# Kernel optimization log

Measured on AMD Instinct MI355X. Metric: run time of the kernel, lower is better.

Reference implementation:

```python
import jax, jax.numpy as jnp
import numpy as np

ALPHA = 0.2  # LeakyReLU negative slope
N_NODES = 50000
N_EDGES = 800000
IN_F = 128
OUT_F = 64


def setup_inputs() -> dict:
    key = jax.random.key(0)
    k1, k2, k3, k4 = jax.random.split(key, 4)
    x = jax.random.normal(k1, (N_NODES, IN_F), dtype=jnp.float32)
    edge_index = jax.random.randint(k2, (2, N_EDGES), 0, N_NODES, dtype=jnp.int64)
    # xavier_uniform-ish scales
    W = jax.random.uniform(k3, (IN_F, OUT_F), dtype=jnp.float32,
                           minval=-1.0, maxval=1.0) * (1.414 * np.sqrt(6.0 / (IN_F + OUT_F)))
    a = jax.random.uniform(k4, (2 * OUT_F, 1), dtype=jnp.float32,
                           minval=-1.0, maxval=1.0) * (1.414 * np.sqrt(6.0 / (2 * OUT_F + 1)))
    return {"x": x, "edge_index": edge_index, "W": W, "a": a}


def reference(x, edge_index, W, a):
    Wh = x @ W                               # [N, F_out]
    src = edge_index[0]
    dst = edge_index[1]
    Wh_src = Wh[src]                         # [E, F_out] gather
    Wh_dst = Wh[dst]                         # [E, F_out] gather
    # concat([Wh_src, Wh_dst]) @ a == Wh_src @ a_top + Wh_dst @ a_bot
    F_out = Wh.shape[1]
    a_top = a[:F_out, 0]
    a_bot = a[F_out:, 0]
    e = jax.nn.leaky_relu(Wh_src @ a_top + Wh_dst @ a_bot, negative_slope=ALPHA)  # [E]
    # NOTE: original normalizes softmax over ALL edges (dim=0), not per node.
    attention = jax.nn.softmax(e)            # [E]
    # dropout skipped (eval mode, deterministic reference)
    msgs = Wh_dst * attention[:, None]       # [E, F_out]
    h_prime = jax.ops.segment_sum(msgs, src, num_segments=Wh.shape[0])  # scatter-add
    return jax.nn.elu(h_prime)
```

## Files before the change

kernel.cpp:

```cpp
#include <hip/hip_runtime.h>
#include <math.h>

#define N_NODES 50000
#define N_EDGES 800000
#define IN_F 128
#define OUT_F 64
#define LRELU_ALPHA 0.2f

#define NPB 64
#define NBUCK ((N_NODES + NPB - 1) / NPB)
#define EPT 16
#define NBT ((N_EDGES / EPT + 255) / 256)
#define CHUNK 2048

typedef __attribute__((ext_vector_type(8))) short bf16x8;
typedef __attribute__((ext_vector_type(4))) float f32x4;

__device__ inline float wred_sum(float v) {
#pragma unroll
    for (int o = 32; o > 0; o >>= 1) v += __shfl_down(v, o, 64);
    return v;
}

__device__ inline unsigned bf16r(float f) {
    unsigned u = __float_as_uint(f);
    u += 0x7fffu + ((u >> 16) & 1u);
    return u >> 16;
}

__global__ __launch_bounds__(256, 4) void k_wh(const float* __restrict__ x,
                                               const float* __restrict__ W,
                                               const float* __restrict__ a,
                                               const int* __restrict__ src,
                                               unsigned short* __restrict__ Whb,
                                               float* __restrict__ sv,
                                               float* __restrict__ tv,
                                               int* __restrict__ bcnt) {
    __shared__ unsigned short xb[64 * 128];
    __shared__ unsigned short wtl[64 * 128];
    __shared__ float wt_s[128], wb_s[128];
    __shared__ int hc[NBUCK];

    const int tid = threadIdx.x;
    const int row0 = blockIdx.x * 64;

    for (int i = tid; i < NBUCK; i += 256) hc[i] = 0;

    for (int i = tid; i < 2048; i += 256) {
        int k = i >> 4, c4 = (i & 15) << 2;
        float4 wv = *reinterpret_cast<const float4*>(W + k * 64 + c4);
        int kb = k >> 3, kr = k & 7;
        wtl[(c4 + 0) * 128 + ((kb ^ ((c4 + 0) & 15)) << 3) + kr] = (unsigned short)bf16r(wv.x);
        wtl[(c4 + 1) * 128 + ((kb ^ ((c4 + 1) & 15)) << 3) + kr] = (unsigned short)bf16r(wv.y);
        wtl[(c4 + 2) * 128 + ((kb ^ ((c4 + 2) & 15)) << 3) + kr] = (unsigned short)bf16r(wv.z);
        wtl[(c4 + 3) * 128 + ((kb ^ ((c4 + 3) & 15)) << 3) + kr] = (unsigned short)bf16r(wv.w);
    }

    if (tid < 128) {
        int k = tid;
        float s = 0.0f, t = 0.0f;
#pragma unroll
        for (int c4 = 0; c4 < 64; c4 += 4) {
            float4 wv = *reinterpret_cast<const float4*>(W + k * 64 + c4);
            float4 at = *reinterpret_cast<const float4*>(a + c4);
            float4 ab = *reinterpret_cast<const float4*>(a + 64 + c4);
            s = fmaf(wv.w, at.w, fmaf(wv.z, at.z, fmaf(wv.y, at.y, fmaf(wv.x, at.x, s))));
            t = fmaf(wv.w, ab.w, fmaf(wv.z, ab.z, fmaf(wv.y, ab.y, fmaf(wv.x, ab.x, t))));
        }
        wt_s[k] = s;
        wb_s[k] = t;
    }

    {
        int j0 = blockIdx.x * 1024 + tid * 4;
        if (j0 < N_EDGES) {
            int4 s4 = *reinterpret_cast<const int4*>(src + j0);
            atomicAdd(&hc[s4.x >> 6], 1);
            atomicAdd(&hc[s4.y >> 6], 1);
            atomicAdd(&hc[s4.z >> 6], 1);
            atomicAdd(&hc[s4.w >> 6], 1);
        }
    }
    __syncthreads();

    const int cc = (tid & 31) << 2;
    float4 wt4 = *reinterpret_cast<const float4*>(wt_s + cc);
    float4 wb4 = *reinterpret_cast<const float4*>(wb_s + cc);
    float ps[8], pt[8];
#pragma unroll
    for (int it = 0; it < 8; ++it) {
        int i = tid + it * 256;
        int rl = i >> 5;
        int r = row0 + rl;
        float4 v = make_float4(0.f, 0.f, 0.f, 0.f);
        if (r < N_NODES) v = *reinterpret_cast<const float4*>(x + (size_t)r * IN_F + cc);
        ps[it] = fmaf(v.w, wt4.w, fmaf(v.z, wt4.z, fmaf(v.y, wt4.y, v.x * wt4.x)));
        pt[it] = fmaf(v.w, wb4.w, fmaf(v.z, wb4.z, fmaf(v.y, wb4.y, v.x * wb4.x)));
        int kb = cc >> 3;
        uint2 pk;
        pk.x = bf16r(v.x) | (bf16r(v.y) << 16);
        pk.y = bf16r(v.z) | (bf16r(v.w) << 16);
        *reinterpret_cast<uint2*>(
            &xb[rl * 128 + (kb ^ (rl & 15)) * 8 + ((cc >> 2) & 1) * 4]) = pk;
    }
    __syncthreads();

    const int l = tid & 63, w = tid >> 6;
    const int rloc0 = w * 16;
    const int arow = rloc0 + (l & 15);
    const int kgrp = l >> 4;
    f32x4 acc[4] = {f32x4{0,0,0,0}, f32x4{0,0,0,0}, f32x4{0,0,0,0}, f32x4{0,0,0,0}};
#pragma unroll
    for (int t = 0; t < 4; ++t) {
        int kb = t * 4 + kgrp;
        bf16x8 af = *reinterpret_cast<const bf16x8*>(
            &xb[arow * 128 + (kb ^ (arow & 15)) * 8]);
#pragma unroll
        for (int ct = 0; ct < 4; ++ct) {
            int brow = ct * 16 + (l & 15);
            bf16x8 bfr = *reinterpret_cast<const bf16x8*>(
                &wtl[brow * 128 + (kb ^ (brow & 15)) * 8]);
            acc[ct] = __builtin_amdgcn_mfma_f32_16x16x32_bf16(af, bfr, acc[ct], 0, 0, 0);
        }
    }

#pragma unroll
    for (int ct = 0; ct < 4; ++ct) {
#pragma unroll
        for (int i = 0; i < 4; ++i) {
            int r = row0 + rloc0 + (l >> 4) * 4 + i;
            if (r < N_NODES)
                Whb[(size_t)r * OUT_F + ct * 16 + (l & 15)] =
                    (unsigned short)bf16r(acc[ct][i]);
        }
    }

#pragma unroll
    for (int it = 0; it < 8; ++it) {
        float s = ps[it], t2 = pt[it];
#pragma unroll
        for (int o = 1; o < 32; o <<= 1) {
            s += __shfl_xor(s, o, 64);
            t2 += __shfl_xor(t2, o, 64);
        }
        int r = row0 + (tid >> 5) + it * 8;
        if ((tid & 31) == 0 && r < N_NODES) { sv[r] = s; tv[r] = t2; }
    }

    for (int i = tid; i < NBUCK; i += 256) {
        int v = hc[i];
        if (v) atomicAdd(&bcnt[i], v);
    }
}

__global__ __launch_bounds__(1024) void k_bscan(const int* __restrict__ bcnt,
                                                int* __restrict__ bbase,
                                                int* __restrict__ cursor) {
    __shared__ int wsum[16], woff[16];
    int t = threadIdx.x, lane = t & 63, w = t >> 6;
    int c = (t < NBUCK) ? bcnt[t] : 0;
    int run = c;
#pragma unroll
    for (int o = 1; o < 64; o <<= 1) {
        int v = __shfl_up(run, o, 64);
        if (lane >= o) run += v;
    }
    if (lane == 63) wsum[w] = run;
    __syncthreads();
    if (t == 0) {
        int r = 0;
#pragma unroll
        for (int i = 0; i < 16; i++) { woff[i] = r; r += wsum[i]; }
    }
    __syncthreads();
    int ex = run - c + woff[w];
    if (t < NBUCK) {
        bbase[t] = ex;
        cursor[t] = ex;
    }
    if (t == 0) bbase[NBUCK] = N_EDGES;
}

__global__ __launch_bounds__(256) void k_binscatter(const int* __restrict__ src,
                                                    const int* __restrict__ dst,
                                                    const float* __restrict__ sv,
                                                    const float* __restrict__ tv,
                                                    int* __restrict__ cursor,
                                                    int2* __restrict__ rec,
                                                    float* __restrict__ psum) {
    __shared__ int lcnt[NBUCK];
    __shared__ int lbase[NBUCK];
    const int tid = threadIdx.x;
    for (int i = tid; i < NBUCK; i += 256) lcnt[i] = 0;
    __syncthreads();

    int t = blockIdx.x * 256 + tid;
    int j0 = t * EPT;
    bool ok = (j0 < N_EDGES);

    int s_[EPT], d_[EPT], rk[EPT];
    float ev[EPT];
    float lsum = 0.0f;
    if (ok) {
#pragma unroll
        for (int q = 0; q < 4; q++) {
            int4 s4 = *reinterpret_cast<const int4*>(src + j0 + q * 4);
            int4 d4 = *reinterpret_cast<const int4*>(dst + j0 + q * 4);
            s_[q * 4 + 0] = s4.x; s_[q * 4 + 1] = s4.y;
            s_[q * 4 + 2] = s4.z; s_[q * 4 + 3] = s4.w;
            d_[q * 4 + 0] = d4.x; d_[q * 4 + 1] = d4.y;
            d_[q * 4 + 2] = d4.z; d_[q * 4 + 3] = d4.w;
        }
        float svv[EPT], tvv[EPT];
#pragma unroll
        for (int k = 0; k < EPT; k++) svv[k] = sv[s_[k]];
#pragma unroll
        for (int k = 0; k < EPT; k++) tvv[k] = tv[d_[k]];
#pragma unroll
        for (int k = 0; k < EPT; k++) {
            float vv = svv[k] + tvv[k];
            vv = vv > 0.0f ? vv : LRELU_ALPHA * vv;
            float e = __expf(vv);
            ev[k] = e;
            lsum += e;
        }
#pragma unroll
        for (int k = 0; k < EPT; k++) rk[k] = atomicAdd(&lcnt[s_[k] >> 6], 1);
    }
    __syncthreads();

    for (int i = tid; i < NBUCK; i += 256) {
        int c = lcnt[i];
        lbase[i] = c ? atomicAdd(&cursor[i], c) : 0;
    }
    __syncthreads();

    if (ok) {
#pragma unroll
        for (int k = 0; k < EPT; k++) {
            int b = s_[k] >> 6;
            rec[lbase[b] + rk[k]] =
                make_int2(d_[k] | ((s_[k] & (NPB - 1)) << 16), __float_as_int(ev[k]));
        }
    }

    float wsum = wred_sum(lsum);
    __shared__ float rsm[4];
    if ((tid & 63) == 0) rsm[tid >> 6] = wsum;
    __syncthreads();
    if (tid == 0)
        psum[blockIdx.x] = rsm[0] + rsm[1] + rsm[2] + rsm[3];
}

__global__ __launch_bounds__(512) void k_bgather(const int* __restrict__ bbase,
                                                 const int2* __restrict__ rec,
                                                 const float* __restrict__ psum,
                                                 const unsigned short* __restrict__ Whb,
                                                 float* __restrict__ out) {
    __shared__ int2 sorted[CHUNK];
    __shared__ int scnt[NPB], soff[NPB], shead[NPB];
    __shared__ float ginv_s;

    const int tid = threadIdx.x;
    const int lane = tid & 63, w = tid >> 6;
    const int j = lane & 31, h = lane >> 5;
    const int b = blockIdx.x;
    const int e0 = bbase[b], e1 = bbase[b + 1];

    if (tid < 64) {
        float lsum = 0.0f;
        for (int i = tid; i < NBT; i += 64) lsum += psum[i];
        float ws = wred_sum(lsum);
        if (tid == 0) ginv_s = 1.0f / ws;
    }
    __syncthreads();
    const float ginv = ginv_s;

    float ax[8], ay[8];
#pragma unroll
    for (int k = 0; k < 8; k++) { ax[k] = 0.0f; ay[k] = 0.0f; }

    for (int base = e0; base < e1; base += CHUNK) {
        int m = e1 - base;
        if (m > CHUNK) m = CHUNK;

        int2 rr[4];
        int ln[4];
        bool vv[4];
        if (tid < NPB) scnt[tid] = 0;
        __syncthreads();
#pragma unroll
        for (int q = 0; q < 4; q++) {
            int idx = tid + q * 512;
            vv[q] = idx < m;
            rr[q] = make_int2(0, 0);
            ln[q] = 0;
            if (vv[q]) {
                rr[q] = rec[base + idx];
                ln[q] = (rr[q].x >> 16) & (NPB - 1);
                atomicAdd(&scnt[ln[q]], 1);
            }
        }
        __syncthreads();

        if (tid < 64) {
            int c = scnt[tid];
            int run = c;
#pragma unroll
            for (int o = 1; o < 64; o <<= 1) {
                int src_ln = (tid >= o) ? (tid - o) : tid;
                int t2 = __shfl(run, src_ln, 64);
                if (tid >= o) run += t2;
            }
            int excl = run - c;
            soff[tid] = excl;
            shead[tid] = excl;
        }
        __syncthreads();

#pragma unroll
        for (int q = 0; q < 4; q++) {
            if (vv[q]) {
                int pos = atomicAdd(&shead[ln[q]], 1);
                sorted[pos] = make_int2(rr[q].x & 0xFFFF, rr[q].y);
            }
        }
        __syncthreads();

#pragma unroll
        for (int k = 0; k < 8; k++) {
            int node = w * 8 + k;
            int lo = soff[node], c = scnt[node];
            float px = 0.0f, py = 0.0f;
            int i = 0;
            for (; i + 7 < c; i += 8) {
                int2 q0 = sorted[lo + i + h];
                int2 q1 = sorted[lo + i + 2 + h];
                int2 q2 = sorted[lo + i + 4 + h];
                int2 q3 = sorted[lo + i + 6 + h];
                const unsigned* p0 =
                    reinterpret_cast<const unsigned*>(Whb + (size_t)q0.x * OUT_F);
                const unsigned* p1 =
                    reinterpret_cast<const unsigned*>(Whb + (size_t)q1.x * OUT_F);
                const unsigned* p2 =
                    reinterpret_cast<const unsigned*>(Whb + (size_t)q2.x * OUT_F);
                const unsigned* p3 =
                    reinterpret_cast<const unsigned*>(Whb + (size_t)q3.x * OUT_F);
                unsigned u0 = p0[j];
                unsigned u1 = p1[j];
                unsigned u2 = p2[j];
                unsigned u3 = p3[j];
                float att0 = __int_as_float(q0.y);
                float att1 = __int_as_float(q1.y);
                float att2 = __int_as_float(q2.y);
                float att3 = __int_as_float(q3.y);
                px = fmaf(att0, __uint_as_float((u0 & 0xffffu) << 16), px);
                py = fmaf(att0, __uint_as_float(u0 & 0xffff0000u), py);
                px = fmaf(att1, __uint_as_float((u1 & 0xffffu) << 16), px);
                py = fmaf(att1, __uint_as_float(u1 & 0xffff0000u), py);
                px = fmaf(att2, __uint_as_float((u2 & 0xffffu) << 16), px);
                py = fmaf(att2, __uint_as_float(u2 & 0xffff0000u), py);
                px = fmaf(att3, __uint_as_float((u3 & 0xffffu) << 16), px);
                py = fmaf(att3, __uint_as_float(u3 & 0xffff0000u), py);
            }
            for (; i < c; i += 2) {
                int ii = i + h;
                bool val = ii < c;
                int2 q = sorted[lo + (val ? ii : i)];
                const unsigned* p =
                    reinterpret_cast<const unsigned*>(Whb + (size_t)q.x * OUT_F);
                unsigned u = p[j];
                float att = val ? __int_as_float(q.y) : 0.0f;
                px = fmaf(att, __uint_as_float((u & 0xffffu) << 16), px);
                py = fmaf(att, __uint_as_float(u & 0xffff0000u), py);
            }
            ax[k] += px;
            ay[k] += py;
        }
        __syncthreads();
    }

#pragma unroll
    for (int k = 0; k < 8; k++) {
        float sx = ax[k] + __shfl_down(ax[k], 32, 64);
        float sy = ay[k] + __shfl_down(ay[k], 32, 64);
        int n = b * NPB + w * 8 + k;
        if (h == 0 && n < N_NODES) {
            float2 v;
            v.x = sx * ginv;
            v.y = sy * ginv;
            v.x = v.x > 0.0f ? v.x : expm1f(v.x);
            v.y = v.y > 0.0f ? v.y : expm1f(v.y);
            *reinterpret_cast<float2*>(out + (size_t)n * OUT_F + 2 * j) = v;
        }
    }
}

extern "C" void kernel_launch(void* const* d_in, const int* in_sizes, int n_in,
                              void* d_out, int out_size, void* d_ws, size_t ws_size,
                              hipStream_t stream) {
    const float* x  = (const float*)d_in[0];
    const int*   ei = (const int*)d_in[1];
    const float* W  = (const float*)d_in[2];
    const float* a  = (const float*)d_in[3];
    float* out = (float*)d_out;

    const int* src = ei;
    const int* dst = ei + N_EDGES;

    unsigned short* Whb = (unsigned short*)d_ws;
    float* sv     = (float*)(Whb + (size_t)N_NODES * OUT_F);
    float* tv     = sv + N_NODES;
    float* psum   = tv + N_NODES;
    int*   bcnt   = (int*)(psum + 512);
    int*   bbase  = bcnt + NBUCK;
    int*   cursor = bbase + NBUCK + 1;
    size_t used = (size_t)((char*)(cursor + NBUCK) - (char*)d_ws);
    used = (used + 15) & ~(size_t)15;
    int2*  rec  = (int2*)((char*)d_ws + used);

    hipMemsetAsync(bcnt, 0, NBUCK * sizeof(int), stream);
    k_wh<<<(N_NODES + 63) / 64, 256, 0, stream>>>(x, W, a, src, Whb, sv, tv, bcnt);
    k_bscan<<<1, 1024, 0, stream>>>(bcnt, bbase, cursor);
    k_binscatter<<<NBT, 256, 0, stream>>>(src, dst, sv, tv, cursor, rec, psum);
    k_bgather<<<NBUCK, 512, 0, stream>>>(bbase, rec, psum, Whb, out);
}
```

Before: 102.2 us.

## Replace atomic bucket histogram with per-block histogram table; tune EPT and gather unroll

Each k_wh block now writes its full bucket histogram into a 2D table instead of atomically adding into a global count, which also removes the memset. The single-block scan kernel then sums every block's row for each bucket before scanning. The edge-scatter kernel drops from 16 to 8 edges per thread. The gather loop gains a 16-wide unrolled path to keep more loads in flight. The cost is that one 1024-thread block must now serially read roughly 600K histogram entries, which may take far longer than the atomics it replaces.

```diff
diff --git a/kernel.cpp b/kernel.cpp
--- a/kernel.cpp
+++ b/kernel.cpp
@@ -9,8 +9,9 @@
 
 #define NPB 64
 #define NBUCK ((N_NODES + NPB - 1) / NPB)
-#define EPT 16
+#define EPT 8
 #define NBT ((N_EDGES / EPT + 255) / 256)
+#define NWH ((N_NODES + 63) / 64)
 #define CHUNK 2048
 
 typedef __attribute__((ext_vector_type(8))) short bf16x8;
@@ -35,7 +36,7 @@
                                                unsigned short* __restrict__ Whb,
                                                float* __restrict__ sv,
                                                float* __restrict__ tv,
-                                               int* __restrict__ bcnt) {
+                                               int* __restrict__ hist2d) {
     __shared__ unsigned short xb[64 * 128];
     __shared__ unsigned short wtl[64 * 128];
     __shared__ float wt_s[128], wb_s[128];
@@ -147,18 +148,26 @@
         if ((tid & 31) == 0 && r < N_NODES) { sv[r] = s; tv[r] = t2; }
     }
 
-    for (int i = tid; i < NBUCK; i += 256) {
-        int v = hc[i];
-        if (v) atomicAdd(&bcnt[i], v);
-    }
-}
-
-__global__ __launch_bounds__(1024) void k_bscan(const int* __restrict__ bcnt,
+    for (int i = tid; i < NBUCK; i += 256)
+        hist2d[(size_t)blockIdx.x * NBUCK + i] = hc[i];
+}
+
+__global__ __launch_bounds__(1024) void k_bscan(const int* __restrict__ hist2d,
                                                 int* __restrict__ bbase,
                                                 int* __restrict__ cursor) {
     __shared__ int wsum[16], woff[16];
     int t = threadIdx.x, lane = t & 63, w = t >> 6;
-    int c = (t < NBUCK) ? bcnt[t] : 0;
+    int c = 0;
+    if (t < NBUCK) {
+        int b = 0;
+        for (; b + 3 < NWH; b += 4) {
+            c += hist2d[(size_t)b * NBUCK + t];
+            c += hist2d[(size_t)(b + 1) * NBUCK + t];
+            c += hist2d[(size_t)(b + 2) * NBUCK + t];
+            c += hist2d[(size_t)(b + 3) * NBUCK + t];
+        }
+        for (; b < NWH; b++) c += hist2d[(size_t)b * NBUCK + t];
+    }
     int run = c;
 #pragma unroll
     for (int o = 1; o < 64; o <<= 1) {
@@ -202,15 +211,14 @@
     float ev[EPT];
     float lsum = 0.0f;
     if (ok) {
-#pragma unroll
-        for (int q = 0; q < 4; q++) {
-            int4 s4 = *reinterpret_cast<const int4*>(src + j0 + q * 4);
-            int4 d4 = *reinterpret_cast<const int4*>(dst + j0 + q * 4);
-            s_[q * 4 + 0] = s4.x; s_[q * 4 + 1] = s4.y;
-            s_[q * 4 + 2] = s4.z; s_[q * 4 + 3] = s4.w;
-            d_[q * 4 + 0] = d4.x; d_[q * 4 + 1] = d4.y;
-            d_[q * 4 + 2] = d4.z; d_[q * 4 + 3] = d4.w;
-        }
+        int4 a4 = *reinterpret_cast<const int4*>(src + j0);
+        int4 b4 = *reinterpret_cast<const int4*>(src + j0 + 4);
+        int4 c4 = *reinterpret_cast<const int4*>(dst + j0);
+        int4 e4 = *reinterpret_cast<const int4*>(dst + j0 + 4);
+        s_[0] = a4.x; s_[1] = a4.y; s_[2] = a4.z; s_[3] = a4.w;
+        s_[4] = b4.x; s_[5] = b4.y; s_[6] = b4.z; s_[7] = b4.w;
+        d_[0] = c4.x; d_[1] = c4.y; d_[2] = c4.z; d_[3] = c4.w;
+        d_[4] = e4.x; d_[5] = e4.y; d_[6] = e4.z; d_[7] = e4.w;
         float svv[EPT], tvv[EPT];
 #pragma unroll
         for (int k = 0; k < EPT; k++) svv[k] = sv[s_[k]];
@@ -333,23 +341,35 @@
             int lo = soff[node], c = scnt[node];
             float px = 0.0f, py = 0.0f;
             int i = 0;
+            for (; i + 15 < c; i += 16) {
+                int2 q_[8];
+#pragma unroll
+                for (int m2 = 0; m2 < 8; m2++) q_[m2] = sorted[lo + i + 2 * m2 + h];
+                unsigned u_[8];
+#pragma unroll
+                for (int m2 = 0; m2 < 8; m2++)
+                    u_[m2] = reinterpret_cast<const unsigned*>(
+                        Whb + (size_t)q_[m2].x * OUT_F)[j];
+#pragma unroll
+                for (int m2 = 0; m2 < 8; m2++) {
+                    float att = __int_as_float(q_[m2].y);
+                    px = fmaf(att, __uint_as_float((u_[m2] & 0xffffu) << 16), px);
+                    py = fmaf(att, __uint_as_float(u_[m2] & 0xffff0000u), py);
+                }
+            }
             for (; i + 7 < c; i += 8) {
                 int2 q0 = sorted[lo + i + h];
                 int2 q1 = sorted[lo + i + 2 + h];
                 int2 q2 = sorted[lo + i + 4 + h];
                 int2 q3 = sorted[lo + i + 6 + h];
-                const unsigned* p0 =
-                    reinterpret_cast<const unsigned*>(Whb + (size_t)q0.x * OUT_F);
-                const unsigned* p1 =
-                    reinterpret_cast<const unsigned*>(Whb + (size_t)q1.x * OUT_F);
-                const unsigned* p2 =
-                    reinterpret_cast<const unsigned*>(Whb + (size_t)q2.x * OUT_F);
-                const unsigned* p3 =
-                    reinterpret_cast<const unsigned*>(Whb + (size_t)q3.x * OUT_F);
-                unsigned u0 = p0[j];
-                unsigned u1 = p1[j];
-                unsigned u2 = p2[j];
-                unsigned u3 = p3[j];
+                unsigned u0 = reinterpret_cast<const unsigned*>(
+                    Whb + (size_t)q0.x * OUT_F)[j];
+                unsigned u1 = reinterpret_cast<const unsigned*>(
+                    Whb + (size_t)q1.x * OUT_F)[j];
+                unsigned u2 = reinterpret_cast<const unsigned*>(
+                    Whb + (size_t)q2.x * OUT_F)[j];
+                unsigned u3 = reinterpret_cast<const unsigned*>(
+                    Whb + (size_t)q3.x * OUT_F)[j];
                 float att0 = __int_as_float(q0.y);
                 float att1 = __int_as_float(q1.y);
                 float att2 = __int_as_float(q2.y);
@@ -367,9 +387,8 @@
                 int ii = i + h;
                 bool val = ii < c;
                 int2 q = sorted[lo + (val ? ii : i)];
-                const unsigned* p =
-                    reinterpret_cast<const unsigned*>(Whb + (size_t)q.x * OUT_F);
-                unsigned u = p[j];
+                unsigned u = reinterpret_cast<const unsigned*>(
+                    Whb + (size_t)q.x * OUT_F)[j];
                 float att = val ? __int_as_float(q.y) : 0.0f;
                 px = fmaf(att, __uint_as_float((u & 0xffffu) << 16), px);
                 py = fmaf(att, __uint_as_float(u & 0xffff0000u), py);
@@ -412,16 +431,17 @@
     float* sv     = (float*)(Whb + (size_t)N_NODES * OUT_F);
     float* tv     = sv + N_NODES;
     float* psum   = tv + N_NODES;
-    int*   bcnt   = (int*)(psum + 512);
-    int*   bbase  = bcnt + NBUCK;
+    int*   bbase  = (int*)(psum + 512);
     int*   cursor = bbase + NBUCK + 1;
     size_t used = (size_t)((char*)(cursor + NBUCK) - (char*)d_ws);
     used = (used + 15) & ~(size_t)15;
+    int*   hist2d = (int*)((char*)d_ws + used);
+    used += (size_t)NWH * NBUCK * sizeof(int);
+    used = (used + 15) & ~(size_t)15;
     int2*  rec  = (int2*)((char*)d_ws + used);
 
-    hipMemsetAsync(bcnt, 0, NBUCK * sizeof(int), stream);
-    k_wh<<<(N_NODES + 63) / 64, 256, 0, stream>>>(x, W, a, src, Whb, sv, tv, bcnt);
-    k_bscan<<<1, 1024, 0, stream>>>(bcnt, bbase, cursor);
+    k_wh<<<NWH, 256, 0, stream>>>(x, W, a, src, Whb, sv, tv, hist2d);
+    k_bscan<<<1, 1024, 0, stream>>>(hist2d, bbase, cursor);
     k_binscatter<<<NBT, 256, 0, stream>>>(src, dst, sv, tv, cursor, rec, psum);
     k_bgather<<<NBUCK, 512, 0, stream>>>(bbase, rec, psum, Whb, out);
 }
```

Result: slower. 118.2 us (+15.7%).

## Split bf16 Wh into two 32-feature halves gathered in separate passes

Applied to the files above, without the earlier changes.

Stores Wh as two planar arrays holding feature columns 0-31 and 32-63, each 64 bytes per row. The gather kernel now makes two passes over the sorted edges, using 16 lanes per row and 4 edges per wavefront step in each pass. The aim is to halve the working set touched per pass so the gathered rows stay in cache better. The cost is reading the shared-memory edge list twice, twice as many accumulators, and an extra shuffle reduction.

```diff
diff --git a/kernel.cpp b/kernel.cpp
--- a/kernel.cpp
+++ b/kernel.cpp
@@ -32,7 +32,8 @@
                                                const float* __restrict__ W,
                                                const float* __restrict__ a,
                                                const int* __restrict__ src,
-                                               unsigned short* __restrict__ Whb,
+                                               unsigned short* __restrict__ Whb_lo,
+                                               unsigned short* __restrict__ Whb_hi,
                                                float* __restrict__ sv,
                                                float* __restrict__ tv,
                                                int* __restrict__ bcnt) {
@@ -129,9 +130,13 @@
 #pragma unroll
         for (int i = 0; i < 4; ++i) {
             int r = row0 + rloc0 + (l >> 4) * 4 + i;
-            if (r < N_NODES)
-                Whb[(size_t)r * OUT_F + ct * 16 + (l & 15)] =
-                    (unsigned short)bf16r(acc[ct][i]);
+            if (r < N_NODES) {
+                unsigned short v = (unsigned short)bf16r(acc[ct][i]);
+                if (ct < 2)
+                    Whb_lo[(size_t)r * 32 + ct * 16 + (l & 15)] = v;
+                else
+                    Whb_hi[(size_t)r * 32 + (ct - 2) * 16 + (l & 15)] = v;
+            }
         }
     }
 
@@ -255,7 +260,8 @@
 __global__ __launch_bounds__(512) void k_bgather(const int* __restrict__ bbase,
                                                  const int2* __restrict__ rec,
                                                  const float* __restrict__ psum,
-                                                 const unsigned short* __restrict__ Whb,
+                                                 const unsigned short* __restrict__ Whb_lo,
+                                                 const unsigned short* __restrict__ Whb_hi,
                                                  float* __restrict__ out) {
     __shared__ int2 sorted[CHUNK];
     __shared__ int scnt[NPB], soff[NPB], shead[NPB];
@@ -263,7 +269,7 @@
 
     const int tid = threadIdx.x;
     const int lane = tid & 63, w = tid >> 6;
-    const int j = lane & 31, h = lane >> 5;
+    const int j2 = lane & 15, qd = lane >> 4;
     const int b = blockIdx.x;
     const int e0 = bbase[b], e1 = bbase[b + 1];
 
@@ -276,9 +282,11 @@
     __syncthreads();
     const float ginv = ginv_s;
 
-    float ax[8], ay[8];
-#pragma unroll
-    for (int k = 0; k < 8; k++) { ax[k] = 0.0f; ay[k] = 0.0f; }
+    float ax[2][8], ay[2][8];
+#pragma unroll
+    for (int p = 0; p < 2; p++)
+#pragma unroll
+        for (int k = 0; k < 8; k++) { ax[p][k] = 0.0f; ay[p][k] = 0.0f; }
 
     for (int base = e0; base < e1; base += CHUNK) {
         int m = e1 - base;
@@ -328,70 +336,63 @@
         __syncthreads();
 
 #pragma unroll
+        for (int p = 0; p < 2; p++) {
+            const unsigned short* Wp = p ? Whb_hi : Whb_lo;
+#pragma unroll
+            for (int k = 0; k < 8; k++) {
+                int node = w * 8 + k;
+                int lo = soff[node], c = scnt[node];
+                float px = 0.0f, py = 0.0f;
+                int i = 0;
+                for (; i + 7 < c; i += 8) {
+                    int2 q0 = sorted[lo + i + qd];
+                    int2 q1 = sorted[lo + i + 4 + qd];
+                    unsigned u0 = reinterpret_cast<const unsigned*>(
+                        Wp + (size_t)q0.x * 32)[j2];
+                    unsigned u1 = reinterpret_cast<const unsigned*>(
+                        Wp + (size_t)q1.x * 32)[j2];
+                    float att0 = __int_as_float(q0.y);
+                    float att1 = __int_as_float(q1.y);
+                    px = fmaf(att0, __uint_as_float((u0 & 0xffffu) << 16), px);
+                    py = fmaf(att0, __uint_as_float(u0 & 0xffff0000u), py);
+                    px = fmaf(att1, __uint_as_float((u1 & 0xffffu) << 16), px);
+                    py = fmaf(att1, __uint_as_float(u1 & 0xffff0000u), py);
+                }
+                for (; i < c; i += 4) {
+                    int ii = i + qd;
+                    bool val = ii < c;
+                    int2 q = sorted[lo + (val ? ii : i)];
+                    unsigned u = reinterpret_cast<const unsigned*>(
+                        Wp + (size_t)q.x * 32)[j2];
+                    float att = val ? __int_as_float(q.y) : 0.0f;
+                    px = fmaf(att, __uint_as_float((u & 0xffffu) << 16), px);
+                    py = fmaf(att, __uint_as_float(u & 0xffff0000u), py);
+                }
+                ax[p][k] += px;
+                ay[p][k] += py;
+            }
+        }
+        __syncthreads();
+    }
+
+#pragma unroll
+    for (int p = 0; p < 2; p++) {
+#pragma unroll
         for (int k = 0; k < 8; k++) {
-            int node = w * 8 + k;
-            int lo = soff[node], c = scnt[node];
-            float px = 0.0f, py = 0.0f;
-            int i = 0;
-            for (; i + 7 < c; i += 8) {
-                int2 q0 = sorted[lo + i + h];
-                int2 q1 = sorted[lo + i + 2 + h];
-                int2 q2 = sorted[lo + i + 4 + h];
-                int2 q3 = sorted[lo + i + 6 + h];
-                const unsigned* p0 =
-                    reinterpret_cast<const unsigned*>(Whb + (size_t)q0.x * OUT_F);
-                const unsigned* p1 =
-                    reinterpret_cast<const unsigned*>(Whb + (size_t)q1.x * OUT_F);
-                const unsigned* p2 =
-                    reinterpret_cast<const unsigned*>(Whb + (size_t)q2.x * OUT_F);
-                const unsigned* p3 =
-                    reinterpret_cast<const unsigned*>(Whb + (size_t)q3.x * OUT_F);
-                unsigned u0 = p0[j];
-                unsigned u1 = p1[j];
-                unsigned u2 = p2[j];
-                unsigned u3 = p3[j];
-                float att0 = __int_as_float(q0.y);
-                float att1 = __int_as_float(q1.y);
-                float att2 = __int_as_float(q2.y);
-                float att3 = __int_as_float(q3.y);
-                px = fmaf(att0, __uint_as_float((u0 & 0xffffu) << 16), px);
-                py = fmaf(att0, __uint_as_float(u0 & 0xffff0000u), py);
-                px = fmaf(att1, __uint_as_float((u1 & 0xffffu) << 16), px);
-                py = fmaf(att1, __uint_as_float(u1 & 0xffff0000u), py);
-                px = fmaf(att2, __uint_as_float((u2 & 0xffffu) << 16), px);
-                py = fmaf(att2, __uint_as_float(u2 & 0xffff0000u), py);
-                px = fmaf(att3, __uint_as_float((u3 & 0xffffu) << 16), px);
-                py = fmaf(att3, __uint_as_float(u3 & 0xffff0000u), py);
-            }
-            for (; i < c; i += 2) {
-                int ii = i + h;
-                bool val = ii < c;
-                int2 q = sorted[lo + (val ? ii : i)];
-                const unsigned* p =
-                    reinterpret_cast<const unsigned*>(Whb + (size_t)q.x * OUT_F);
-                unsigned u = p[j];
-                float att = val ? __int_as_float(q.y) : 0.0f;
-                px = fmaf(att, __uint_as_float((u & 0xffffu) << 16), px);
-                py = fmaf(att, __uint_as_float(u & 0xffff0000u), py);
-            }
-            ax[k] += px;
-            ay[k] += py;
-        }
-        __syncthreads();
-    }
-
-#pragma unroll
-    for (int k = 0; k < 8; k++) {
-        float sx = ax[k] + __shfl_down(ax[k], 32, 64);
-        float sy = ay[k] + __shfl_down(ay[k], 32, 64);
-        int n = b * NPB + w * 8 + k;
-        if (h == 0 && n < N_NODES) {
-            float2 v;
-            v.x = sx * ginv;
-            v.y = sy * ginv;
-            v.x = v.x > 0.0f ? v.x : expm1f(v.x);
-            v.y = v.y > 0.0f ? v.y : expm1f(v.y);
-            *reinterpret_cast<float2*>(out + (size_t)n * OUT_F + 2 * j) = v;
+            float sx = ax[p][k] + __shfl_down(ax[p][k], 32, 64);
+            sx += __shfl_down(sx, 16, 64);
+            float sy = ay[p][k] + __shfl_down(ay[p][k], 32, 64);
+            sy += __shfl_down(sy, 16, 64);
+            int n = b * NPB + w * 8 + k;
+            if (qd == 0 && n < N_NODES) {
+                float2 v;
+                v.x = sx * ginv;
+                v.y = sy * ginv;
+                v.x = v.x > 0.0f ? v.x : expm1f(v.x);
+                v.y = v.y > 0.0f ? v.y : expm1f(v.y);
+                *reinterpret_cast<float2*>(
+                    out + (size_t)n * OUT_F + p * 32 + 2 * j2) = v;
+            }
         }
     }
 }
@@ -408,8 +409,9 @@
     const int* src = ei;
     const int* dst = ei + N_EDGES;
 
-    unsigned short* Whb = (unsigned short*)d_ws;
-    float* sv     = (float*)(Whb + (size_t)N_NODES * OUT_F);
+    unsigned short* Whb_lo = (unsigned short*)d_ws;
+    unsigned short* Whb_hi = Whb_lo + (size_t)N_NODES * 32;
+    float* sv     = (float*)(Whb_hi + (size_t)N_NODES * 32);
     float* tv     = sv + N_NODES;
     float* psum   = tv + N_NODES;
     int*   bcnt   = (int*)(psum + 512);
@@ -420,8 +422,9 @@
     int2*  rec  = (int2*)((char*)d_ws + used);
 
     hipMemsetAsync(bcnt, 0, NBUCK * sizeof(int), stream);
-    k_wh<<<(N_NODES + 63) / 64, 256, 0, stream>>>(x, W, a, src, Whb, sv, tv, bcnt);
+    k_wh<<<(N_NODES + 63) / 64, 256, 0, stream>>>(x, W, a, src, Whb_lo, Whb_hi,
+                                                  sv, tv, bcnt);
     k_bscan<<<1, 1024, 0, stream>>>(bcnt, bbase, cursor);
     k_binscatter<<<NBT, 256, 0, stream>>>(src, dst, sv, tv, cursor, rec, psum);
-    k_bgather<<<NBUCK, 512, 0, stream>>>(bbase, rec, psum, Whb, out);
-}
+    k_bgather<<<NBUCK, 512, 0, stream>>>(bbase, rec, psum, Whb_lo, Whb_hi, out);
+}
```

Measured after the change: 166.3 us. +62.7%, slower.
